# Performance work log

Measured on AMD Instinct MI355X. Metric: run time of the kernel, lower is better.

## Reference

```python
import jax, jax.numpy as jnp
import numpy as np
from jax import lax

DIM = 64
HEADS = 2
BATCH, H, W = 4, 192, 192


def _conv1x1(x, w, b=None):
    # x: [b,c,h,w], w: [o,c]
    y = jnp.einsum('bchw,oc->bohw', x, w)
    if b is not None:
        y = y + b[None, :, None, None]
    return y


def _gelu(x):
    return jax.nn.gelu(x, approximate=False)  # torch nn.GELU default (erf)


def setup_inputs() -> dict:
    key = jax.random.key(0)
    ks = jax.random.split(key, 25)
    C = DIM
    n = lambda k, s, scale=0.05: jax.random.normal(k, s, dtype=jnp.float32) * scale
    return {
        'x': jax.random.normal(ks[0], (BATCH, C, H, W), dtype=jnp.float32),
        # BSConvU: pointwise (no bias) + depthwise 3x3 (bias)
        'pw_w': n(ks[1], (C, C)),
        'dw_w': n(ks[2], (C, 1, 3, 3)),
        'dw_b': n(ks[3], (C,)),
        'conv2_w': n(ks[4], (C, C)), 'conv2_b': n(ks[5], (C,)),
        'conv0_w': n(ks[6], (C, C)), 'conv0_b': n(ks[7], (C,)),
        # SelfAttention (bias=False)
        'att_q_w': n(ks[8], (C, C)), 'att_k_w': n(ks[9], (C, C)),
        'att_v_w': n(ks[10], (C, C)), 'att_proj_w': n(ks[11], (C, C)),
        'temperature': jnp.ones((HEADS, 1, 1), dtype=jnp.float32),
        # RowAttention (bias=False)
        'row_q_w': n(ks[12], (C, C)), 'row_k_w': n(ks[13], (C, C)),
        'row_v_w': n(ks[14], (C, C)),
        'row_gamma': n(ks[15], (1,), 0.5),
        # ColAttention (bias=False)
        'col_q_w': n(ks[16], (C, C)), 'col_k_w': n(ks[17], (C, C)),
        'col_v_w': n(ks[18], (C, C)),
        'col_gamma': n(ks[19], (1,), 0.5),
        # final fuse conv: in=3C, out=C
        'conv_w': n(ks[20], (C, 3 * C)), 'conv_b': n(ks[21], (C,)),
    }


def reference(x, pw_w, dw_w, dw_b, conv2_w, conv2_b, conv0_w, conv0_b,
              att_q_w, att_k_w, att_v_w, att_proj_w, temperature,
              row_q_w, row_k_w, row_v_w, row_gamma,
              col_q_w, col_k_w, col_v_w, col_gamma,
              conv_w, conv_b):
    b, c, h, w = x.shape
    # --- BSConvU -> GELU -> conv_2, plus conv_0 skip ---
    t = _conv1x1(x, pw_w)
    t = lax.conv_general_dilated(
        t, dw_w, window_strides=(1, 1), padding=((1, 1), (1, 1)),
        feature_group_count=c,
        dimension_numbers=('NCHW', 'OIHW', 'NCHW')) + dw_b[None, :, None, None]
    x1 = _conv1x1(_gelu(t), conv2_w, conv2_b) + _conv1x1(x, conv0_w, conv0_b)

    # --- channel self-attention (out_1) ---
    ch = c // HEADS
    q = _conv1x1(x1, att_q_w).reshape(b, HEADS, ch, h * w)
    k = _conv1x1(x1, att_k_w).reshape(b, HEADS, ch, h * w)
    v = _conv1x1(x1, att_v_w).reshape(b, HEADS, ch, h * w)
    q = q / jnp.maximum(jnp.linalg.norm(q, axis=-1, keepdims=True), 1e-12)
    k = k / jnp.maximum(jnp.linalg.norm(k, axis=-1, keepdims=True), 1e-12)
    attn = jnp.einsum('bgcn,bgdn->bgcd', q, k) * temperature[None]
    attn = jax.nn.softmax(attn, axis=-1)
    out1 = jnp.einsum('bgcd,bgdn->bgcn', attn, v).reshape(b, c, h, w)
    out1 = _conv1x1(out1, att_proj_w)

    # --- row attention over width, per (batch,row) (out_2) ---
    Q = _conv1x1(x1, row_q_w)
    K = _conv1x1(x1, row_k_w)
    V = _conv1x1(out1, row_v_w)
    s = jnp.einsum('bchi,bchj->bhij', Q, K)         # [b,h,w,w]
    a = jax.nn.softmax(s, axis=-1)
    out2 = jnp.einsum('bchj,bhij->bchi', V, a)
    out2 = row_gamma * out2 + x1

    # --- col attention over height, per (batch,col) (out_3) ---
    Q = _conv1x1(x1, col_q_w)
    K = _conv1x1(x1, col_k_w)
    V = _conv1x1(out1, col_v_w)
    s = jnp.einsum('bciw,bcjw->bwij', Q, K)         # [b,w,h,h]
    a = jax.nn.softmax(s, axis=-1)
    out3 = jnp.einsum('bcjw,bwij->bciw', V, a)
    out3 = col_gamma * out3 + x1

    out = jnp.concatenate([out1, out2, out3], axis=1)
    return _gelu(_conv1x1(out, conv_w, conv_b))
```

## Files before the change

### kernel.cpp

```cpp
#include <hip/hip_runtime.h>
#include <cstdio>

#define BB 4
#define C 64
#define HH 192
#define WW 192
#define NPIX (HH*WW)
#define ST (BB*C*NPIX)

__device__ __forceinline__ float gelu_f(float v) {
    return 0.5f * v * (1.0f + erff(v * 0.70710678118654752440f));
}

typedef __fp16 h2 __attribute__((ext_vector_type(2)));

__device__ __forceinline__ h2 pkh2(float lo, float hi) {
#if __has_builtin(__builtin_amdgcn_cvt_pkrtz)
    return __builtin_amdgcn_cvt_pkrtz(lo, hi);
#else
    h2 r; r[0] = (__fp16)lo; r[1] = (__fp16)hi; return r;
#endif
}

__device__ __forceinline__ float dot2f(h2 a, h2 b, float c) {
#if __has_builtin(__builtin_amdgcn_fdot2)
    return __builtin_amdgcn_fdot2(a, b, c, false);
#else
    return c + (float)a[0]*(float)b[0] + (float)a[1]*(float)b[1];
#endif
}

__device__ __forceinline__ void ld4h2(const void* p, h2* d) {
    const float4 f = *reinterpret_cast<const float4*>(p);
    d[0] = __builtin_bit_cast(h2, f.x);
    d[1] = __builtin_bit_cast(h2, f.y);
    d[2] = __builtin_bit_cast(h2, f.z);
    d[3] = __builtin_bit_cast(h2, f.w);
}

template<bool TWO_IN, bool PERB, bool DO_GELU>
__global__ __launch_bounds__(256, 3) void k_gconv(
    const float* __restrict__ in1, const float* __restrict__ in2,
    const float* __restrict__ W1, const float* __restrict__ W2,
    const float* __restrict__ bias1, const float* __restrict__ bias2,
    float* __restrict__ out, int ldw1, int ldw2)
{
    extern __shared__ float sm[];
    float* Wl = sm;
    float* Xl = sm + 4352;
    const int t = threadIdx.x;
    const int px0 = blockIdx.x * 128;
    const int b = blockIdx.y;
    const size_t base = (size_t)b*(C*NPIX) + px0;
    const int to = t >> 5, tp = t & 31;
    const int o0 = to*8, p0 = tp*4;
    float acc[8][4];
#pragma unroll
    for (int k = 0; k < 8; ++k) {
        float bo = 0.f;
        if (bias1) bo += bias1[o0+k];
        if (bias2) bo += bias2[o0+k];
#pragma unroll
        for (int m = 0; m < 4; ++m) acc[k][m] = bo;
    }
    const int NIN = TWO_IN ? 2 : 1;
#pragma unroll
    for (int inp = 0; inp < NIN; ++inp) {
        const float* In = inp ? in2 : in1;
        const float* Wk = inp ? W2 : (PERB ? W1 + b*4096 : W1);
        const int ldw = inp ? ldw2 : ldw1;
#pragma unroll
        for (int k = 0; k < 16; ++k) {
            const int idx = k*256 + t;
            const int o = idx >> 6, c = idx & 63;
            Wl[c*68 + o] = Wk[o*ldw + c];
        }
#pragma unroll
        for (int k = 0; k < 8; ++k) {
            const int f4 = k*256 + t;
            const int c = f4 >> 5, p4 = (f4 & 31)*4;
            *reinterpret_cast<float4*>(&Xl[c*132 + p4]) =
                *reinterpret_cast<const float4*>(&In[base + (size_t)c*NPIX + p4]);
        }
        __syncthreads();
#pragma unroll 2
        for (int c = 0; c < 64; ++c) {
            const float4 wa = *reinterpret_cast<const float4*>(&Wl[c*68 + o0]);
            const float4 wb = *reinterpret_cast<const float4*>(&Wl[c*68 + o0 + 4]);
            const float4 xv = *reinterpret_cast<const float4*>(&Xl[c*132 + p0]);
            const float wr[8] = {wa.x,wa.y,wa.z,wa.w, wb.x,wb.y,wb.z,wb.w};
            const float xr[4] = {xv.x,xv.y,xv.z,xv.w};
#pragma unroll
            for (int k = 0; k < 8; ++k)
#pragma unroll
                for (int m = 0; m < 4; ++m) acc[k][m] += wr[k]*xr[m];
        }
        __syncthreads();
    }
#pragma unroll
    for (int k = 0; k < 8; ++k) {
        float4 o4;
        if (DO_GELU) {
            o4.x = gelu_f(acc[k][0]); o4.y = gelu_f(acc[k][1]);
            o4.z = gelu_f(acc[k][2]); o4.w = gelu_f(acc[k][3]);
        } else {
            o4.x = acc[k][0]; o4.y = acc[k][1];
            o4.z = acc[k][2]; o4.w = acc[k][3];
        }
        *reinterpret_cast<float4*>(&out[base + (size_t)(o0+k)*NPIX + p0]) = o4;
    }
}

__global__ __launch_bounds__(256, 3) void k_conv4(
    const float* __restrict__ i1, const float* __restrict__ i2,
    const float* __restrict__ i3, const float* __restrict__ i4,
    const float* __restrict__ W1, const float* __restrict__ W2,
    const float* __restrict__ W3, const float* __restrict__ W4,
    const float* __restrict__ bias, float* __restrict__ out)
{
    extern __shared__ float sm[];
    float* Wl = sm;
    float* Xl = sm + 4352;
    const int t = threadIdx.x;
    const int px0 = blockIdx.x * 128;
    const int b = blockIdx.y;
    const size_t base = (size_t)b*(C*NPIX) + px0;
    const int to = t >> 5, tp = t & 31;
    const int o0 = to*8, p0 = tp*4;
    float acc[8][4];
#pragma unroll
    for (int k = 0; k < 8; ++k) {
        const float bo = bias[o0+k];
#pragma unroll
        for (int m = 0; m < 4; ++m) acc[k][m] = bo;
    }
#pragma unroll
    for (int inp = 0; inp < 4; ++inp) {
        const float* In = (inp==0)?i1:(inp==1)?i2:(inp==2)?i3:i4;
        const float* Wk = (inp==0)?W1:(inp==1)?W2:(inp==2)?W3:W4;
        const int ldw = (inp==0)?192:64;
#pragma unroll
        for (int k = 0; k < 16; ++k) {
            const int idx = k*256 + t;
            const int o = idx >> 6, c = idx & 63;
            Wl[c*68 + o] = Wk[o*ldw + c];
        }
#pragma unroll
        for (int k = 0; k < 8; ++k) {
            const int f4 = k*256 + t;
            const int c = f4 >> 5, p4 = (f4 & 31)*4;
            *reinterpret_cast<float4*>(&Xl[c*132 + p4]) =
                *reinterpret_cast<const float4*>(&In[base + (size_t)c*NPIX + p4]);
        }
        __syncthreads();
#pragma unroll 2
        for (int c = 0; c < 64; ++c) {
            const float4 wa = *reinterpret_cast<const float4*>(&Wl[c*68 + o0]);
            const float4 wb = *reinterpret_cast<const float4*>(&Wl[c*68 + o0 + 4]);
            const float4 xv = *reinterpret_cast<const float4*>(&Xl[c*132 + p0]);
            const float wr[8] = {wa.x,wa.y,wa.z,wa.w, wb.x,wb.y,wb.z,wb.w};
            const float xr[4] = {xv.x,xv.y,xv.z,xv.w};
#pragma unroll
            for (int k = 0; k < 8; ++k)
#pragma unroll
                for (int m = 0; m < 4; ++m) acc[k][m] += wr[k]*xr[m];
        }
        __syncthreads();
    }
#pragma unroll
    for (int k = 0; k < 8; ++k) {
        float4 o4;
        o4.x = gelu_f(acc[k][0]); o4.y = gelu_f(acc[k][1]);
        o4.z = gelu_f(acc[k][2]); o4.w = gelu_f(acc[k][3]);
        *reinterpret_cast<float4*>(&out[base + (size_t)(o0+k)*NPIX + p0]) = o4;
    }
}

__global__ __launch_bounds__(192) void k_dw(
    const float* __restrict__ t0, const float* __restrict__ w,
    const float* __restrict__ bias, float* __restrict__ g)
{
    const int x = threadIdx.x;
    const int y = blockIdx.x;
    const int bc = blockIdx.y;
    const int c = bc & 63;
    const float* img = t0 + bc * NPIX;
    const float* wc = w + c * 9;
    float acc = bias[c];
#pragma unroll
    for (int dy = -1; dy <= 1; ++dy) {
        const int yy = y + dy;
        if (yy < 0 || yy > 191) continue;
#pragma unroll
        for (int dx = -1; dx <= 1; ++dx) {
            const int xx = x + dx;
            if (xx < 0 || xx > 191) continue;
            acc += img[yy*WW + xx] * wc[(dy+1)*3 + (dx+1)];
        }
    }
    g[bc*NPIX + y*WW + x] = gelu_f(acc);
}

__global__ __launch_bounds__(256) void k_gram_part(
    const float* __restrict__ x1p, float* __restrict__ part)
{
    extern __shared__ float lt[];
    const int chunk = blockIdx.x, b = blockIdx.y, t = threadIdx.x;
    const int gbase = b * (C*NPIX) + chunk * 256;
    for (int idx = t; idx < C*256; idx += 256) {
        const int c = idx >> 8, n = idx & 255;
        lt[n*68 + c] = x1p[gbase + c*NPIX + n];
    }
    __syncthreads();
    const int ti = t & 15, tj = t >> 4;
    float acc[4][4];
#pragma unroll
    for (int r = 0; r < 4; ++r)
#pragma unroll
        for (int s = 0; s < 4; ++s) acc[r][s] = 0.f;
    for (int n = 0; n < 256; ++n) {
        const float4 av = *reinterpret_cast<const float4*>(&lt[n*68 + 4*ti]);
        const float4 bv = *reinterpret_cast<const float4*>(&lt[n*68 + 4*tj]);
        const float ar[4] = {av.x, av.y, av.z, av.w};
        const float br[4] = {bv.x, bv.y, bv.z, bv.w};
#pragma unroll
        for (int r = 0; r < 4; ++r)
#pragma unroll
            for (int s = 0; s < 4; ++s) acc[r][s] += ar[r] * br[s];
    }
    float* pb = part + (b*144 + chunk)*4096;
#pragma unroll
    for (int r = 0; r < 4; ++r)
#pragma unroll
        for (int s = 0; s < 4; ++s) pb[(4*ti+r)*64 + (4*tj+s)] = acc[r][s];
}

__global__ __launch_bounds__(256) void k_gram_reduce(
    const float* __restrict__ part, float* __restrict__ G1)
{
    const int flat = blockIdx.x*256 + threadIdx.x;
    const int b = flat >> 12, ij = flat & 4095;
    float s = 0.f;
    for (int ch = 0; ch < 144; ++ch) s += part[(b*144+ch)*4096 + ij];
    G1[flat] = s;
}

__global__ __launch_bounds__(256) void k_attn_small(
    const float* __restrict__ G1a, const float* __restrict__ Wq,
    const float* __restrict__ Wk, const float* __restrict__ Wv,
    const float* __restrict__ Wp, const float* __restrict__ temp,
    float* __restrict__ M2)
{
    extern __shared__ float sm[];
    float* g1 = sm;
    float* wa = sm + 4096;
    float* wb = sm + 8192;
    float* u  = sm + 12288;
    float* at = sm + 16384;
    float* nq = sm + 18432;
    float* nk = sm + 18496;
    const int b = blockIdx.x, t = threadIdx.x;
    const float* G = G1a + b*4096;
    for (int i = t; i < 4096; i += 256) { g1[i] = G[i]; wa[i] = Wq[i]; wb[i] = Wk[i]; }
    __syncthreads();
    {
        const int r = t >> 2, q4 = t & 3;
        for (int cc = q4*16; cc < q4*16 + 16; ++cc) {
            float s = 0.f;
            for (int k = 0; k < 64; ++k) s += wa[r*64+k] * g1[k*64+cc];
            u[r*64+cc] = s;
        }
    }
    __syncthreads();
    {
        const int d = t >> 2, kq = t & 3;
        float p = 0.f;
        for (int k = kq*16; k < kq*16 + 16; ++k) {
            float tk = 0.f;
            for (int c2 = 0; c2 < 64; ++c2) tk += g1[k*64+c2] * wb[d*64+c2];
            p += wb[d*64+k] * tk;
        }
        p += __shfl_xor(p, 1);
        p += __shfl_xor(p, 2);
        if (kq == 0) nk[d] = sqrtf(fmaxf(p, 0.f));
    }
    if (t < 64) {
        float s = 0.f;
        for (int c2 = 0; c2 < 64; ++c2) s += u[t*64+c2] * wa[t*64+c2];
        nq[t] = sqrtf(fmaxf(s, 0.f));
    }
    __syncthreads();
    if (t < 64) {
        const int gI = t >> 5;
        const float tg = temp[gI];
        const float dq = fmaxf(nq[t], 1e-12f);
        float row[32];
        float mx = -1e30f;
#pragma unroll
        for (int d2 = 0; d2 < 32; ++d2) {
            const int dd = gI*32 + d2;
            float s = 0.f;
            for (int c2 = 0; c2 < 64; ++c2) s += u[t*64+c2] * wb[dd*64+c2];
            s = s * tg / (dq * fmaxf(nk[dd], 1e-12f));
            row[d2] = s; mx = fmaxf(mx, s);
        }
        float se = 0.f;
#pragma unroll
        for (int d2 = 0; d2 < 32; ++d2) { row[d2] = __expf(row[d2]-mx); se += row[d2]; }
        const float inv = 1.f / se;
#pragma unroll
        for (int d2 = 0; d2 < 32; ++d2) at[t*32+d2] = row[d2]*inv;
    }
    __syncthreads();
    for (int i = t; i < 4096; i += 256) { wa[i] = Wv[i]; wb[i] = Wp[i]; }
    __syncthreads();
    {
        const int m = t >> 2, q4 = t & 3, gI = m >> 5;
        for (int e = q4*16; e < q4*16 + 16; ++e) {
            float s = 0.f;
#pragma unroll
            for (int d2 = 0; d2 < 32; ++d2) s += at[m*32+d2] * wa[(gI*32+d2)*64 + e];
            g1[m*64+e] = s;
        }
    }
    __syncthreads();
    {
        const int o = t >> 2, q4 = t & 3;
        for (int e = q4*16; e < q4*16 + 16; ++e) {
            float s = 0.f;
            for (int m = 0; m < 64; ++m) s += wb[o*64+m] * g1[m*64+e];
            M2[b*4096 + o*64+e] = s;
        }
    }
}

__global__ __launch_bounds__(256) void k_small_mats(
    const float* __restrict__ rq, const float* __restrict__ rk,
    const float* __restrict__ cq, const float* __restrict__ ck,
    const float* __restrict__ fw, const float* __restrict__ rv,
    const float* __restrict__ cv, const float* __restrict__ rg,
    const float* __restrict__ cg,
    float* __restrict__ Wtr, float* __restrict__ Wtc,
    float* __restrict__ Wf2p, float* __restrict__ Wf3p,
    float* __restrict__ Wfx)
{
    const int which = blockIdx.x, t = threadIdx.x;
    const int a = t >> 2, b0 = (t & 3) * 16;
    if (which <= 1) {
        const float* Q = which ? cq : rq;
        const float* Kw = which ? ck : rk;
        float* O = which ? Wtc : Wtr;
        for (int b = b0; b < b0 + 16; ++b) {
            float s = 0.f;
            for (int co = 0; co < 64; ++co) s += Q[co*64 + a] * Kw[co*64 + b];
            O[a*64 + b] = s;
        }
    } else if (which <= 3) {
        const float* Vw = (which == 2) ? rv : cv;
        const float g = (which == 2) ? rg[0] : cg[0];
        const int off = (which == 2) ? 64 : 128;
        float* O = (which == 2) ? Wf2p : Wf3p;
        for (int b = b0; b < b0 + 16; ++b) {
            float s = 0.f;
            for (int m = 0; m < 64; ++m) s += fw[a*192 + off + m] * Vw[m*64 + b];
            O[a*64 + b] = g * s;
        }
    } else {
        for (int b = b0; b < b0 + 16; ++b)
            Wfx[a*64 + b] = fw[a*192 + 64 + b] + fw[a*192 + 128 + b];
    }
}

#define SP 196
#define PSTR 100
template<bool COLMAJ>
__global__ __launch_bounds__(256, 2) void k_attn_fused(
    const float* __restrict__ X, const float* __restrict__ Wt,
    const float* __restrict__ U, float* __restrict__ Z)
{
    extern __shared__ float sm[];
    h2* Xh = reinterpret_cast<h2*>(sm);
    h2* Yh = reinterpret_cast<h2*>(sm + 6272);
    h2* Ph = reinterpret_cast<h2*>(sm);
    float* red  = sm;
    float* mrow = sm + 3264;
    float* lrow = sm + 19200;
    const int t = threadIdx.x;
    const int h = blockIdx.x, b = blockIdx.y;
    const size_t gbase = (size_t)b*(C*NPIX) + (size_t)h*WW;

    if (COLMAJ) {
        const size_t cbase = (size_t)b*(C*NPIX) + h;
#pragma unroll 4
        for (int k = 0; k < 24; ++k) {
            const int idx = k*256 + t;
            const int cc = idx / 192, j = idx - cc*192;
            const size_t a0 = cbase + (size_t)(2*cc)*NPIX + (size_t)j*WW;
            Xh[cc*SP + j] = pkh2(X[a0], X[a0 + NPIX]);
        }
    } else {
#pragma unroll
        for (int k = 0; k < 6; ++k) {
            const int idx = k*256 + t;
            const int cc = idx / 48, jg = (idx - cc*48) * 4;
            const float4 lo = *reinterpret_cast<const float4*>(
                &X[gbase + (size_t)(2*cc)*NPIX + jg]);
            const float4 hi = *reinterpret_cast<const float4*>(
                &X[gbase + (size_t)(2*cc+1)*NPIX + jg]);
            float4 o;
            o.x = __builtin_bit_cast(float, pkh2(lo.x, hi.x));
            o.y = __builtin_bit_cast(float, pkh2(lo.y, hi.y));
            o.z = __builtin_bit_cast(float, pkh2(lo.z, hi.z));
            o.w = __builtin_bit_cast(float, pkh2(lo.w, hi.w));
            *reinterpret_cast<float4*>(&Xh[cc*SP + jg]) = o;
        }
    }
    __syncthreads();

    {
        const int tc = t & 15, tjy = t >> 4;
        const int c0 = 4*tc, j0y = 12*tjy;
        float accy[4][12];
#pragma unroll
        for (int k = 0; k < 4; ++k)
#pragma unroll
            for (int m = 0; m < 12; ++m) accy[k][m] = 0.f;
        for (int aa = 0; aa < 32; ++aa) {
            const float4 wlo = *reinterpret_cast<const float4*>(&Wt[(2*aa)*64 + c0]);
            const float4 whi = *reinterpret_cast<const float4*>(&Wt[(2*aa+1)*64 + c0]);
            h2 wh[4];
            wh[0] = pkh2(wlo.x, whi.x); wh[1] = pkh2(wlo.y, whi.y);
            wh[2] = pkh2(wlo.z, whi.z); wh[3] = pkh2(wlo.w, whi.w);
            h2 xh[12];
            ld4h2(&Xh[aa*SP + j0y],     xh);
            ld4h2(&Xh[aa*SP + j0y + 4], xh+4);
            ld4h2(&Xh[aa*SP + j0y + 8], xh+8);
#pragma unroll
            for (int k = 0; k < 4; ++k)
#pragma unroll
                for (int m = 0; m < 12; ++m)
                    accy[k][m] = dot2f(wh[k], xh[m], accy[k][m]);
        }
#pragma unroll
        for (int m = 0; m < 12; ++m) {
            Yh[(2*tc)*SP + j0y + m]   = pkh2(accy[0][m], accy[1][m]);
            Yh[(2*tc+1)*SP + j0y + m] = pkh2(accy[2][m], accy[3][m]);
        }
    }
    __syncthreads();

    const int ti = t & 15, tj = t >> 4;
    const int i0 = ti*12, j0 = tj*12;
    float acc[12][12];
#pragma unroll
    for (int r = 0; r < 12; ++r)
#pragma unroll
        for (int s = 0; s < 12; ++s) acc[r][s] = 0.f;
#pragma unroll 2
    for (int cc = 0; cc < 32; ++cc) {
        h2 xh[12], yh[12];
        ld4h2(&Xh[cc*SP + i0],     xh);
        ld4h2(&Xh[cc*SP + i0 + 4], xh+4);
        ld4h2(&Xh[cc*SP + i0 + 8], xh+8);
        ld4h2(&Yh[cc*SP + j0],     yh);
        ld4h2(&Yh[cc*SP + j0 + 4], yh+4);
        ld4h2(&Yh[cc*SP + j0 + 8], yh+8);
#pragma unroll
        for (int r = 0; r < 12; ++r)
#pragma unroll
            for (int s = 0; s < 12; ++s)
                acc[r][s] = dot2f(xh[r], yh[s], acc[r][s]);
    }
    __syncthreads();

#pragma unroll
    for (int r = 0; r < 12; ++r) {
        float pm = acc[r][0];
#pragma unroll
        for (int s = 1; s < 12; ++s) pm = fmaxf(pm, acc[r][s]);
        red[(i0 + r)*17 + tj] = pm;
    }
    __syncthreads();
    if (t < 192) {
        float m = red[t*17];
#pragma unroll
        for (int k = 1; k < 16; ++k) m = fmaxf(m, red[t*17 + k]);
        mrow[t] = m;
    }
    __syncthreads();
#pragma unroll
    for (int r = 0; r < 12; ++r) {
        const float mi = mrow[i0 + r];
        float ps = 0.f;
#pragma unroll
        for (int s = 0; s < 12; ++s) {
            acc[r][s] = __expf(acc[r][s] - mi);
            ps += acc[r][s];
        }
        red[(i0 + r)*17 + tj] = ps;
    }
    __syncthreads();
    if (t < 192) {
        float l = 0.f;
#pragma unroll
        for (int k = 0; k < 16; ++k) l += red[t*17 + k];
        lrow[t] = 1.f / l;
    }
    __syncthreads();

    {
        const int jh0 = j0 >> 1;
#pragma unroll
        for (int r = 0; r < 12; ++r)
#pragma unroll
            for (int q = 0; q < 6; ++q)
                Ph[(i0 + r)*PSTR + jh0 + q] = pkh2(acc[r][2*q], acc[r][2*q+1]);
    }
    __syncthreads();

    const int ci = t & 15, ii = t >> 4;
    const int c0z = 4*ci, i0z = 12*ii;
    const float* Ub = U + gbase;
    float accz[4][12];
#pragma unroll
    for (int k = 0; k < 4; ++k)
#pragma unroll
        for (int m = 0; m < 12; ++m) accz[k][m] = 0.f;
    for (int jt = 0; jt < 192; jt += 8) {
        h2 uh[4][4];
#pragma unroll
        for (int k = 0; k < 4; ++k) {
            const float4 ua = *reinterpret_cast<const float4*>(&Ub[(size_t)(c0z+k)*NPIX + jt]);
            const float4 ub = *reinterpret_cast<const float4*>(&Ub[(size_t)(c0z+k)*NPIX + jt + 4]);
            uh[k][0] = pkh2(ua.x, ua.y); uh[k][1] = pkh2(ua.z, ua.w);
            uh[k][2] = pkh2(ub.x, ub.y); uh[k][3] = pkh2(ub.z, ub.w);
        }
        h2 ph[12][4];
#pragma unroll
        for (int m = 0; m < 12; ++m)
            ld4h2(&Ph[(i0z+m)*PSTR + (jt >> 1)], ph[m]);
#pragma unroll
        for (int k = 0; k < 4; ++k)
#pragma unroll
            for (int m = 0; m < 12; ++m) {
                float a = accz[k][m];
                a = dot2f(uh[k][0], ph[m][0], a);
                a = dot2f(uh[k][1], ph[m][1], a);
                a = dot2f(uh[k][2], ph[m][2], a);
                a = dot2f(uh[k][3], ph[m][3], a);
                accz[k][m] = a;
            }
    }
    float lr[12];
#pragma unroll
    for (int m = 0; m < 12; ++m) lr[m] = lrow[i0z + m];
#pragma unroll
    for (int k = 0; k < 4; ++k) {
        float* zr = Z + gbase + (size_t)(c0z + k)*NPIX + i0z;
        float4 o0, o1, o2;
        o0.x = accz[k][0]*lr[0]; o0.y = accz[k][1]*lr[1];  o0.z = accz[k][2]*lr[2];   o0.w = accz[k][3]*lr[3];
        o1.x = accz[k][4]*lr[4]; o1.y = accz[k][5]*lr[5];  o1.z = accz[k][6]*lr[6];   o1.w = accz[k][7]*lr[7];
        o2.x = accz[k][8]*lr[8]; o2.y = accz[k][9]*lr[9];  o2.z = accz[k][10]*lr[10]; o2.w = accz[k][11]*lr[11];
        *reinterpret_cast<float4*>(zr)     = o0;
        *reinterpret_cast<float4*>(zr + 4) = o1;
        *reinterpret_cast<float4*>(zr + 8) = o2;
    }
}

__global__ __launch_bounds__(256) void k_transpose(
    const float* __restrict__ in, float* __restrict__ out)
{
    __shared__ float tile[32][33];
    const int tx = threadIdx.x & 31, ty = threadIdx.x >> 5;
    const int x0 = blockIdx.x*32, y0 = blockIdx.y*32;
    const float* img = in + blockIdx.z * NPIX;
    float* og = out + blockIdx.z * NPIX;
#pragma unroll
    for (int r = ty; r < 32; r += 8) tile[r][tx] = img[(y0+r)*WW + x0+tx];
    __syncthreads();
#pragma unroll
    for (int r = ty; r < 32; r += 8) og[(x0+r)*WW + (y0+tx)] = tile[tx][r];
}

extern "C" void kernel_launch(void* const* d_in, const int* in_sizes, int n_in,
                              void* d_out, int out_size, void* d_ws, size_t ws_size,
                              hipStream_t stream) {
    const float* x       = (const float*)d_in[0];
    const float* pw_w    = (const float*)d_in[1];
    const float* dw_w    = (const float*)d_in[2];
    const float* dw_b    = (const float*)d_in[3];
    const float* conv2_w = (const float*)d_in[4];
    const float* conv2_b = (const float*)d_in[5];
    const float* conv0_w = (const float*)d_in[6];
    const float* conv0_b = (const float*)d_in[7];
    const float* attq    = (const float*)d_in[8];
    const float* attk    = (const float*)d_in[9];
    const float* attv    = (const float*)d_in[10];
    const float* attp    = (const float*)d_in[11];
    const float* temp    = (const float*)d_in[12];
    const float* rq      = (const float*)d_in[13];
    const float* rk      = (const float*)d_in[14];
    const float* rv      = (const float*)d_in[15];
    const float* rg      = (const float*)d_in[16];
    const float* cq      = (const float*)d_in[17];
    const float* ck      = (const float*)d_in[18];
    const float* cv      = (const float*)d_in[19];
    const float* cg      = (const float*)d_in[20];
    const float* fw      = (const float*)d_in[21];
    const float* fb      = (const float*)d_in[22];

    float* ws = (float*)d_ws;
    float* A  = ws;
    float* Bf = ws + (size_t)ST;
    float* Cf = ws + 2*(size_t)ST;
    float* Df = ws + 3*(size_t)ST;
    float* Ef = ws + 4*(size_t)ST;
    float* partials = ws + 5*(size_t)ST;
    float* G1 = partials + 576*4096;
    float* M2 = G1 + 16384;
    float* Wtr  = M2 + 16384;
    float* Wtc  = Wtr + 4096;
    float* Wf2p = Wtc + 4096;
    float* Wf3p = Wf2p + 4096;
    float* Wfx  = Wf3p + 4096;

    const size_t need = ((size_t)5*ST + 576*4096 + 16384 + 16384 + 5*4096)
                        * sizeof(float);
    if (ws_size < need) {
        fprintf(stderr, "kernel_launch: ws_size %zu < needed %zu\n", ws_size, need);
        return;
    }

    (void)hipFuncSetAttribute((const void*)k_gram_part,
        hipFuncAttributeMaxDynamicSharedMemorySize, 69632);
    (void)hipFuncSetAttribute((const void*)k_attn_small,
        hipFuncAttributeMaxDynamicSharedMemorySize, 74240);
    (void)hipFuncSetAttribute((const void*)(k_attn_fused<false>),
        hipFuncAttributeMaxDynamicSharedMemorySize, 77568);
    (void)hipFuncSetAttribute((const void*)(k_attn_fused<true>),
        hipFuncAttributeMaxDynamicSharedMemorySize, 77568);
    (void)hipFuncSetAttribute((const void*)k_conv4,
        hipFuncAttributeMaxDynamicSharedMemorySize, 51200);
    (void)hipFuncSetAttribute((const void*)(k_gconv<false,false,false>),
        hipFuncAttributeMaxDynamicSharedMemorySize, 51200);
    (void)hipFuncSetAttribute((const void*)(k_gconv<true,false,false>),
        hipFuncAttributeMaxDynamicSharedMemorySize, 51200);
    (void)hipFuncSetAttribute((const void*)(k_gconv<false,true,false>),
        hipFuncAttributeMaxDynamicSharedMemorySize, 51200);

    const dim3 blk256(256), blk192(192);
    const dim3 gconv(NPIX/128, BB);
    const dim3 ggram(NPIX/256, BB);
    const dim3 gline(HH, BB);
    const dim3 gtr(6, 6, BB*C);

    k_small_mats<<<dim3(5), blk256, 0, stream>>>(rq, rk, cq, ck, fw, rv, cv,
                                                 rg, cg, Wtr, Wtc, Wf2p, Wf3p, Wfx);
    k_gconv<false,false,false><<<gconv, blk256, 51200, stream>>>(
        x, nullptr, pw_w, nullptr, nullptr, nullptr, A, 64, 64);
    k_dw<<<dim3(HH, BB*C), blk192, 0, stream>>>(A, dw_w, dw_b, Bf);
    k_gconv<true,false,false><<<gconv, blk256, 51200, stream>>>(
        Bf, x, conv2_w, conv0_w, conv2_b, conv0_b, A, 64, 64);
    k_gram_part<<<ggram, blk256, 69632, stream>>>(A, partials);
    k_gram_reduce<<<dim3(64), blk256, 0, stream>>>(partials, G1);
    k_attn_small<<<dim3(BB), blk256, 74240, stream>>>(G1, attq, attk, attv, attp, temp, M2);
    k_gconv<false,true,false><<<gconv, blk256, 51200, stream>>>(
        A, nullptr, M2, nullptr, nullptr, nullptr, Bf, 64, 64);
    k_transpose<<<gtr, blk256, 0, stream>>>(Bf, Df);
    k_attn_fused<true><<<gline, blk256, 77568, stream>>>(A, Wtc, Df, Ef);
    k_transpose<<<gtr, blk256, 0, stream>>>(Ef, Df);
    k_attn_fused<false><<<gline, blk256, 77568, stream>>>(A, Wtr, Bf, Cf);
    k_conv4<<<gconv, blk256, 51200, stream>>>(
        Bf, Cf, Df, A, fw, Wf2p, Wf3p, Wfx, fb, (float*)d_out);
}
```

Baseline: 829.3 us.

## Pre-transpose x1 during the Gram pass and fuse the output transpose into row attention

```diff
diff --git a/kernel.cpp b/kernel.cpp
--- a/kernel.cpp
+++ b/kernel.cpp
@@ -36,6 +36,18 @@
     d[1] = __builtin_bit_cast(h2, f.y);
     d[2] = __builtin_bit_cast(h2, f.z);
     d[3] = __builtin_bit_cast(h2, f.w);
+}
+
+__device__ __forceinline__ void tr_tile(const float* __restrict__ img,
+                                        float* __restrict__ og,
+                                        int x0, int y0, int t, float* tile)
+{
+    const int tx = t & 31, ty = t >> 5;
+#pragma unroll
+    for (int r = ty; r < 32; r += 8) tile[r*33 + tx] = img[(y0+r)*WW + x0+tx];
+    __syncthreads();
+#pragma unroll
+    for (int r = ty; r < 32; r += 8) og[(x0+r)*WW + (y0+tx)] = tile[tx*33 + r];
 }
 
 template<bool TWO_IN, bool PERB, bool DO_GELU>
@@ -201,38 +213,47 @@
     g[bc*NPIX + y*WW + x] = gelu_f(acc);
 }
 
-__global__ __launch_bounds__(256) void k_gram_part(
-    const float* __restrict__ x1p, float* __restrict__ part)
+__global__ __launch_bounds__(256) void k_gram_tr(
+    const float* __restrict__ x1p, float* __restrict__ part,
+    float* __restrict__ tout)
 {
     extern __shared__ float lt[];
-    const int chunk = blockIdx.x, b = blockIdx.y, t = threadIdx.x;
-    const int gbase = b * (C*NPIX) + chunk * 256;
-    for (int idx = t; idx < C*256; idx += 256) {
-        const int c = idx >> 8, n = idx & 255;
-        lt[n*68 + c] = x1p[gbase + c*NPIX + n];
-    }
-    __syncthreads();
-    const int ti = t & 15, tj = t >> 4;
-    float acc[4][4];
-#pragma unroll
-    for (int r = 0; r < 4; ++r)
-#pragma unroll
-        for (int s = 0; s < 4; ++s) acc[r][s] = 0.f;
-    for (int n = 0; n < 256; ++n) {
-        const float4 av = *reinterpret_cast<const float4*>(&lt[n*68 + 4*ti]);
-        const float4 bv = *reinterpret_cast<const float4*>(&lt[n*68 + 4*tj]);
-        const float ar[4] = {av.x, av.y, av.z, av.w};
-        const float br[4] = {bv.x, bv.y, bv.z, bv.w};
+    const int bid = blockIdx.x, t = threadIdx.x;
+    if (bid < 576) {
+        const int chunk = bid % 144, b = bid / 144;
+        const int gbase = b * (C*NPIX) + chunk * 256;
+        for (int idx = t; idx < C*256; idx += 256) {
+            const int c = idx >> 8, n = idx & 255;
+            lt[n*68 + c] = x1p[gbase + c*NPIX + n];
+        }
+        __syncthreads();
+        const int ti = t & 15, tj = t >> 4;
+        float acc[4][4];
 #pragma unroll
         for (int r = 0; r < 4; ++r)
 #pragma unroll
-            for (int s = 0; s < 4; ++s) acc[r][s] += ar[r] * br[s];
-    }
-    float* pb = part + (b*144 + chunk)*4096;
-#pragma unroll
-    for (int r = 0; r < 4; ++r)
-#pragma unroll
-        for (int s = 0; s < 4; ++s) pb[(4*ti+r)*64 + (4*tj+s)] = acc[r][s];
+            for (int s = 0; s < 4; ++s) acc[r][s] = 0.f;
+        for (int n = 0; n < 256; ++n) {
+            const float4 av = *reinterpret_cast<const float4*>(&lt[n*68 + 4*ti]);
+            const float4 bv = *reinterpret_cast<const float4*>(&lt[n*68 + 4*tj]);
+            const float ar[4] = {av.x, av.y, av.z, av.w};
+            const float br[4] = {bv.x, bv.y, bv.z, bv.w};
+#pragma unroll
+            for (int r = 0; r < 4; ++r)
+#pragma unroll
+                for (int s = 0; s < 4; ++s) acc[r][s] += ar[r] * br[s];
+        }
+        float* pb = part + (b*144 + chunk)*4096;
+#pragma unroll
+        for (int r = 0; r < 4; ++r)
+#pragma unroll
+            for (int s = 0; s < 4; ++s) pb[(4*ti+r)*64 + (4*tj+s)] = acc[r][s];
+    } else {
+        const int tb = bid - 576;
+        const int z = tb / 36, rem = tb % 36;
+        const int x0 = (rem % 6) * 32, y0 = (rem / 6) * 32;
+        tr_tile(x1p + (size_t)z*NPIX, tout + (size_t)z*NPIX, x0, y0, t, lt);
+    }
 }
 
 __global__ __launch_bounds__(256) void k_gram_reduce(
@@ -373,47 +394,33 @@
 
 #define SP 196
 #define PSTR 100
-template<bool COLMAJ>
-__global__ __launch_bounds__(256, 2) void k_attn_fused(
+__device__ __forceinline__ void attn_body(
     const float* __restrict__ X, const float* __restrict__ Wt,
-    const float* __restrict__ U, float* __restrict__ Z)
-{
-    extern __shared__ float sm[];
+    const float* __restrict__ U, float* __restrict__ Z,
+    int h, int b, int t, float* sm)
+{
     h2* Xh = reinterpret_cast<h2*>(sm);
     h2* Yh = reinterpret_cast<h2*>(sm + 6272);
     h2* Ph = reinterpret_cast<h2*>(sm);
     float* red  = sm;
     float* mrow = sm + 3264;
     float* lrow = sm + 19200;
-    const int t = threadIdx.x;
-    const int h = blockIdx.x, b = blockIdx.y;
     const size_t gbase = (size_t)b*(C*NPIX) + (size_t)h*WW;
 
-    if (COLMAJ) {
-        const size_t cbase = (size_t)b*(C*NPIX) + h;
-#pragma unroll 4
-        for (int k = 0; k < 24; ++k) {
-            const int idx = k*256 + t;
-            const int cc = idx / 192, j = idx - cc*192;
-            const size_t a0 = cbase + (size_t)(2*cc)*NPIX + (size_t)j*WW;
-            Xh[cc*SP + j] = pkh2(X[a0], X[a0 + NPIX]);
-        }
-    } else {
-#pragma unroll
-        for (int k = 0; k < 6; ++k) {
-            const int idx = k*256 + t;
-            const int cc = idx / 48, jg = (idx - cc*48) * 4;
-            const float4 lo = *reinterpret_cast<const float4*>(
-                &X[gbase + (size_t)(2*cc)*NPIX + jg]);
-            const float4 hi = *reinterpret_cast<const float4*>(
-                &X[gbase + (size_t)(2*cc+1)*NPIX + jg]);
-            float4 o;
-            o.x = __builtin_bit_cast(float, pkh2(lo.x, hi.x));
-            o.y = __builtin_bit_cast(float, pkh2(lo.y, hi.y));
-            o.z = __builtin_bit_cast(float, pkh2(lo.z, hi.z));
-            o.w = __builtin_bit_cast(float, pkh2(lo.w, hi.w));
-            *reinterpret_cast<float4*>(&Xh[cc*SP + jg]) = o;
-        }
+#pragma unroll
+    for (int k = 0; k < 6; ++k) {
+        const int idx = k*256 + t;
+        const int cc = idx / 48, jg = (idx - cc*48) * 4;
+        const float4 lo = *reinterpret_cast<const float4*>(
+            &X[gbase + (size_t)(2*cc)*NPIX + jg]);
+        const float4 hi = *reinterpret_cast<const float4*>(
+            &X[gbase + (size_t)(2*cc+1)*NPIX + jg]);
+        float4 o;
+        o.x = __builtin_bit_cast(float, pkh2(lo.x, hi.x));
+        o.y = __builtin_bit_cast(float, pkh2(lo.y, hi.y));
+        o.z = __builtin_bit_cast(float, pkh2(lo.z, hi.z));
+        o.w = __builtin_bit_cast(float, pkh2(lo.w, hi.w));
+        *reinterpret_cast<float4*>(&Xh[cc*SP + jg]) = o;
     }
     __syncthreads();
 
@@ -567,19 +574,37 @@
     }
 }
 
+__global__ __launch_bounds__(256, 2) void k_attn_fused(
+    const float* __restrict__ X, const float* __restrict__ Wt,
+    const float* __restrict__ U, float* __restrict__ Z)
+{
+    extern __shared__ float sm[];
+    attn_body(X, Wt, U, Z, blockIdx.x, blockIdx.y, threadIdx.x, sm);
+}
+
+__global__ __launch_bounds__(256, 2) void k_attn_row_tr(
+    const float* __restrict__ X, const float* __restrict__ Wt,
+    const float* __restrict__ U, float* __restrict__ Z,
+    const float* __restrict__ tin, float* __restrict__ tout)
+{
+    extern __shared__ float sm[];
+    const int bid = blockIdx.x, t = threadIdx.x;
+    if (bid < 768) {
+        attn_body(X, Wt, U, Z, bid % 192, bid / 192, t, sm);
+    } else {
+        const int tb = bid - 768;
+        const int z = tb / 36, rem = tb % 36;
+        const int x0 = (rem % 6) * 32, y0 = (rem / 6) * 32;
+        tr_tile(tin + (size_t)z*NPIX, tout + (size_t)z*NPIX, x0, y0, t, sm);
+    }
+}
+
 __global__ __launch_bounds__(256) void k_transpose(
     const float* __restrict__ in, float* __restrict__ out)
 {
-    __shared__ float tile[32][33];
-    const int tx = threadIdx.x & 31, ty = threadIdx.x >> 5;
-    const int x0 = blockIdx.x*32, y0 = blockIdx.y*32;
-    const float* img = in + blockIdx.z * NPIX;
-    float* og = out + blockIdx.z * NPIX;
-#pragma unroll
-    for (int r = ty; r < 32; r += 8) tile[r][tx] = img[(y0+r)*WW + x0+tx];
-    __syncthreads();
-#pragma unroll
-    for (int r = ty; r < 32; r += 8) og[(x0+r)*WW + (y0+tx)] = tile[tx][r];
+    __shared__ float tile[32*33];
+    tr_tile(in + (size_t)blockIdx.z*NPIX, out + (size_t)blockIdx.z*NPIX,
+            blockIdx.x*32, blockIdx.y*32, threadIdx.x, tile);
 }
 
 extern "C" void kernel_launch(void* const* d_in, const int* in_sizes, int n_in,
@@ -631,13 +656,13 @@
         return;
     }
 
-    (void)hipFuncSetAttribute((const void*)k_gram_part,
+    (void)hipFuncSetAttribute((const void*)k_gram_tr,
         hipFuncAttributeMaxDynamicSharedMemorySize, 69632);
     (void)hipFuncSetAttribute((const void*)k_attn_small,
         hipFuncAttributeMaxDynamicSharedMemorySize, 74240);
-    (void)hipFuncSetAttribute((const void*)(k_attn_fused<false>),
+    (void)hipFuncSetAttribute((const void*)k_attn_fused,
         hipFuncAttributeMaxDynamicSharedMemorySize, 77568);
-    (void)hipFuncSetAttribute((const void*)(k_attn_fused<true>),
+    (void)hipFuncSetAttribute((const void*)k_attn_row_tr,
         hipFuncAttributeMaxDynamicSharedMemorySize, 77568);
     (void)hipFuncSetAttribute((const void*)k_conv4,
         hipFuncAttributeMaxDynamicSharedMemorySize, 51200);
@@ -650,7 +675,6 @@
 
     const dim3 blk256(256), blk192(192);
     const dim3 gconv(NPIX/128, BB);
-    const dim3 ggram(NPIX/256, BB);
     const dim3 gline(HH, BB);
     const dim3 gtr(6, 6, BB*C);
 
@@ -661,15 +685,15 @@
     k_dw<<<dim3(HH, BB*C), blk192, 0, stream>>>(A, dw_w, dw_b, Bf);
     k_gconv<true,false,false><<<gconv, blk256, 51200, stream>>>(
         Bf, x, conv2_w, conv0_w, conv2_b, conv0_b, A, 64, 64);
-    k_gram_part<<<ggram, blk256, 69632, stream>>>(A, partials);
+    k_gram_tr<<<dim3(576 + 9216), blk256, 69632, stream>>>(A, partials, Cf);
     k_gram_reduce<<<dim3(64), blk256, 0, stream>>>(partials, G1);
     k_attn_small<<<dim3(BB), blk256, 74240, stream>>>(G1, attq, attk, attv, attp, temp, M2);
     k_gconv<false,true,false><<<gconv, blk256, 51200, stream>>>(
         A, nullptr, M2, nullptr, nullptr, nullptr, Bf, 64, 64);
     k_transpose<<<gtr, blk256, 0, stream>>>(Bf, Df);
-    k_attn_fused<true><<<gline, blk256, 77568, stream>>>(A, Wtc, Df, Ef);
-    k_transpose<<<gtr, blk256, 0, stream>>>(Ef, Df);
-    k_attn_fused<false><<<gline, blk256, 77568, stream>>>(A, Wtr, Bf, Cf);
+    k_attn_fused<<<gline, blk256, 77568, stream>>>(Cf, Wtc, Df, Ef);
+    k_attn_row_tr<<<dim3(768 + 9216), blk256, 77568, stream>>>(
+        A, Wtr, Bf, Cf, Ef, Df);
     k_conv4<<<gconv, blk256, 51200, stream>>>(
         Bf, Cf, Df, A, fw, Wf2p, Wf3p, Wfx, fb, (float*)d_out);
 }
```

After: 812.5 us. 1.02x faster.
